# Performance work log

Hardware: AMD Instinct MI355X
Metric: run time of the kernel (lower is better)

Reference implementation:

```python
import jax, jax.numpy as jnp
import numpy as np

EMBED_DIM = 1024
HEADS = 16


def setup_inputs() -> dict:
    key = jax.random.key(0)
    ks = jax.random.split(key, 9)
    d = EMBED_DIM
    s = 1.0 / np.sqrt(d)
    x = jax.random.normal(ks[0], (4, 2048, d), dtype=jnp.float32)
    return {
        "x": x,
        "Wq": jax.random.uniform(ks[1], (d, d), jnp.float32, -s, s),
        "bq": jax.random.uniform(ks[2], (d,), jnp.float32, -s, s),
        "Wk": jax.random.uniform(ks[3], (d, d), jnp.float32, -s, s),
        "bk": jax.random.uniform(ks[4], (d,), jnp.float32, -s, s),
        "Wv": jax.random.uniform(ks[5], (d, d), jnp.float32, -s, s),
        "bv": jax.random.uniform(ks[6], (d,), jnp.float32, -s, s),
        "Wo": jax.random.uniform(ks[7], (d, d), jnp.float32, -s, s),
        "bo": jax.random.uniform(ks[8], (d,), jnp.float32, -s, s),
    }


def reference(x, Wq, bq, Wk, bk, Wv, bv, Wo, bo):
    B, N, C = x.shape
    H = HEADS
    Dh = C // H
    scale = Dh ** (-0.5)
    # Linear projections (torch Linear: x @ W.T + b), split heads -> [B,H,N,Dh]
    def split_heads(t):
        return t.reshape(B, N, H, Dh).transpose(0, 2, 1, 3)
    q = split_heads(x @ Wq.T + bq)
    k = split_heads(x @ Wk.T + bk)
    v = split_heads(x @ Wv.T + bv)
    attn = jnp.einsum('bhnd,bhmd->bhnm', q, k) * scale  # [B,H,N,N]
    attn = jax.nn.softmax(attn, axis=-1)
    # dropout ratio is 0.0 (eval); abs() kept for faithfulness
    out = jnp.einsum('bhnm,bhmd->bhnd', jnp.abs(attn), v)
    out = out.transpose(0, 2, 1, 3).reshape(B, N, C)
    return out @ Wo.T + bo
```

## Files before the change

kernel.cpp:

```cpp
#include <hip/hip_runtime.h>
#include <hip/hip_bf16.h>
#include <cstddef>
#include <cstdint>

namespace {
constexpr int Bn = 4, SEQ = 2048, CDIM = 1024, NH = 16, DH = 64;
constexpr int Mrows = Bn * SEQ;
}

using bf16x8 = __attribute__((ext_vector_type(8))) __bf16;
using f32x4  = __attribute__((ext_vector_type(4))) float;
using f32x16 = __attribute__((ext_vector_type(16))) float;

#define MFMA16(a, b, c) __builtin_amdgcn_mfma_f32_16x16x32_bf16(a, b, c, 0, 0, 0)
#define MFMA32(a, b, c) __builtin_amdgcn_mfma_f32_32x32x16_bf16(a, b, c, 0, 0, 0)

__device__ __forceinline__ void gload_lds16(const __bf16* g, __bf16* l) {
  __builtin_amdgcn_global_load_lds(
      (const __attribute__((address_space(1))) void*)g,
      (__attribute__((address_space(3))) void*)l, 16, 0, 0);
}

__device__ __forceinline__ unsigned pk2(float a, float b) {
  union { __bf16 h[2]; unsigned u; } x;
  x.h[0] = (__bf16)a; x.h[1] = (__bf16)b;
  return x.u;
}

__global__ __launch_bounds__(256) void cast_inputs(
    const float* __restrict__ x, const float* __restrict__ wq,
    const float* __restrict__ wk, const float* __restrict__ wv,
    const float* __restrict__ wo, __bf16* __restrict__ xb,
    __bf16* __restrict__ wall) {
  constexpr int X4 = Mrows * CDIM / 4;
  constexpr int W4 = CDIM * CDIM / 4;
  constexpr int total = X4 + 4 * W4;
  for (int i = blockIdx.x * 256 + threadIdx.x; i < total; i += gridDim.x * 256) {
    const float4* src;
    __bf16* dst;
    int o;
    if (i < X4) {
      src = (const float4*)x; dst = xb; o = i;
    } else {
      int j = i - X4;
      int w = j >> 18;
      o = j & (W4 - 1);
      src = (const float4*)(w == 0 ? wq : w == 1 ? wk : w == 2 ? wv : wo);
      dst = wall + (size_t)w * (CDIM * CDIM);
    }
    float4 v = src[o];
    union { __bf16 h[4]; ushort4 u4; } pk;
    pk.h[0] = (__bf16)v.x; pk.h[1] = (__bf16)v.y;
    pk.h[2] = (__bf16)v.z; pk.h[3] = (__bf16)v.w;
    *(ushort4*)(dst + (size_t)o * 4) = pk.u4;
  }
}

template <int MODE>
__global__ __launch_bounds__(256) void gemm_mfma(
    const __bf16* __restrict__ A, const __bf16* __restrict__ Bw,
    const float* __restrict__ b0, const float* __restrict__ b1,
    const float* __restrict__ b2, __bf16* __restrict__ Qb,
    __bf16* __restrict__ Kb, __bf16* __restrict__ Vb,
    float* __restrict__ Yf) {
  __shared__ __align__(16) __bf16 As[128 * 32];
  __shared__ __align__(16) __bf16 Bs[128 * 32];
  const int tid = threadIdx.x;
  const int lane = tid & 63, w = tid >> 6;
  const int wr = w >> 1, wc = w & 1;
  const int l4 = lane >> 4, l15 = lane & 15;
  const int m0 = blockIdx.y * 128, n0 = blockIdx.x * 128;

  f32x4 acc[4][4] = {};
  const int srow = lane >> 2;
  const int scol = (lane & 3) * 8;

  for (int k0 = 0; k0 < CDIM; k0 += 32) {
    __syncthreads();
#pragma unroll
    for (int u = 0; u < 2; ++u) {
      const int c = w * 2 + u;
      gload_lds16(A + (size_t)(m0 + c * 16 + srow) * CDIM + k0 + scol,
                  &As[c * 512]);
      gload_lds16(Bw + (size_t)(n0 + c * 16 + srow) * CDIM + k0 + scol,
                  &Bs[c * 512]);
    }
    __syncthreads();
    bf16x8 af[4], bfr[4];
#pragma unroll
    for (int i = 0; i < 4; ++i)
      af[i] = *(const bf16x8*)&As[(wr * 64 + i * 16 + l15) * 32 + l4 * 8];
#pragma unroll
    for (int j = 0; j < 4; ++j)
      bfr[j] = *(const bf16x8*)&Bs[(wc * 64 + j * 16 + l15) * 32 + l4 * 8];
#pragma unroll
    for (int i = 0; i < 4; ++i)
#pragma unroll
      for (int j = 0; j < 4; ++j)
        acc[i][j] = MFMA16(af[i], bfr[j], acc[i][j]);
  }

  const int row0 = m0 + wr * 64;
  if (MODE == 0) {
#pragma unroll
    for (int j = 0; j < 4; ++j) {
      const int n = (n0 + wc * 64 + j * 16) + l15;
      const float bias = b0[n];
#pragma unroll
      for (int i = 0; i < 4; ++i) {
        const int mrow = row0 + i * 16 + l4 * 4;
#pragma unroll
        for (int r = 0; r < 4; ++r)
          Yf[(size_t)(mrow + r) * CDIM + n] = acc[i][j][r] + bias;
      }
    }
  } else {
    const int which = n0 >> 10;
    const float* bias = which == 0 ? b0 : which == 1 ? b1 : b2;
    __bf16* Out = which == 0 ? Qb : which == 1 ? Kb : Vb;
    const float scl = which == 0 ? 0.125f : 1.0f;
    const int n0c = n0 & 1023;
#pragma unroll
    for (int j = 0; j < 4; ++j) {
      const int c = n0c + wc * 64 + j * 16 + l15;
      const int h = c >> 6, dh = c & 63;
      const float bias_v = bias[c];
#pragma unroll
      for (int i = 0; i < 4; ++i) {
        const int mrow = row0 + i * 16 + l4 * 4;
#pragma unroll
        for (int r = 0; r < 4; ++r) {
          const int m = mrow + r;
          const int b_ = m >> 11, ns = m & (SEQ - 1);
          Out[((size_t)(b_ * NH + h) * SEQ + ns) * DH + dh] =
              (__bf16)((acc[i][j][r] + bias_v) * scl);
        }
      }
    }
  }
}

__global__ __launch_bounds__(256) void attn_mfma(
    const __bf16* __restrict__ Qg, const __bf16* __restrict__ Kg,
    const __bf16* __restrict__ Vg, __bf16* __restrict__ AO) {
  __shared__ __align__(16) __bf16 vT[2][64][72];
  const int tid = threadIdx.x, lane = tid & 63, w = tid >> 6;
  const int l31 = lane & 31, hi = lane >> 5;
  const int bh = blockIdx.x, qt = blockIdx.y;
  const int b_ = bh >> 4, h_ = bh & 15;

  const __bf16* Qp = Qg + ((size_t)bh * SEQ + qt * 128 + w * 32) * DH;
  const __bf16* Kb = Kg + (size_t)bh * SEQ * DH;
  const __bf16* Vb = Vg + (size_t)bh * SEQ * DH;

  bf16x8 q[4];
#pragma unroll
  for (int t = 0; t < 4; ++t)
    q[t] = *(const bf16x8*)(Qp + (size_t)l31 * DH + t * 16 + hi * 8);

  f32x16 o0 = {}, o1 = {};
  float m_i = -1e30f, l_i = 0.f;

  const int vkey = tid & 63, vdg = (tid >> 6) * 16;

  bf16x8 kfA[8], kfB[8];
  bf16x8 vfA[2], vfB[2];
  auto kload = [&](bf16x8(&kf)[8], int kt) {
#pragma unroll
    for (int c = 0; c < 2; ++c)
#pragma unroll
      for (int t = 0; t < 4; ++t)
        kf[c * 4 + t] = *(const bf16x8*)(
            Kb + ((size_t)kt * 64 + c * 32 + l31) * DH + t * 16 + hi * 8);
  };
  auto vload = [&](bf16x8(&vf)[2], int kt) {
    const __bf16* Vt = Vb + (size_t)kt * 64 * DH;
    vf[0] = *(const bf16x8*)(Vt + (size_t)vkey * DH + vdg);
    vf[1] = *(const bf16x8*)(Vt + (size_t)vkey * DH + vdg + 8);
  };
  kload(kfA, 0);
  vload(vfA, 0);

  auto body = [&](bf16x8(&kc)[8], bf16x8(&kn)[8], bf16x8(&vc)[2],
                  bf16x8(&vn)[2], int kt, int buf) {
    const int ktn = (kt + 1) & 31;
    vload(vn, ktn);
    kload(kn, ktn);
    f32x16 s0 = {}, s1 = {};
    __builtin_amdgcn_s_setprio(1);
#pragma unroll
    for (int t = 0; t < 4; ++t) {
      s0 = MFMA32(kc[t], q[t], s0);
      s1 = MFMA32(kc[4 + t], q[t], s1);
    }
    __builtin_amdgcn_s_setprio(0);
#pragma unroll
    for (int e = 0; e < 8; ++e) vT[buf][vdg + e][vkey] = vc[0][e];
#pragma unroll
    for (int e = 0; e < 8; ++e) vT[buf][vdg + 8 + e][vkey] = vc[1][e];
    __syncthreads();
    float mt[16];
#pragma unroll
    for (int j = 0; j < 16; ++j) mt[j] = fmaxf(s0[j], s1[j]);
#pragma unroll
    for (int st = 8; st > 0; st >>= 1)
#pragma unroll
      for (int j = 0; j < 8; ++j)
        if (j < st) mt[j] = fmaxf(mt[j], mt[j + st]);
    float mx = fmaxf(mt[0], __shfl_xor(mt[0], 32));
    if (!__all(mx <= m_i + 8.0f)) {
      const float mnew = fmaxf(m_i, mx);
      const float alpha = __expf(m_i - mnew);
      m_i = mnew;
      l_i *= alpha;
      o0 *= alpha;
      o1 *= alpha;
    }
    unsigned W0[4][2], W1[4][2];
    float psa[4] = {0.f, 0.f, 0.f, 0.f};
#pragma unroll
    for (int m = 0; m < 4; ++m)
#pragma unroll
      for (int j2 = 0; j2 < 2; ++j2) {
        float a0 = __expf(s0[4 * m + 2 * j2] - m_i);
        float a1 = __expf(s0[4 * m + 2 * j2 + 1] - m_i);
        float b0 = __expf(s1[4 * m + 2 * j2] - m_i);
        float b1 = __expf(s1[4 * m + 2 * j2 + 1] - m_i);
        psa[m] += (a0 + a1) + (b0 + b1);
        W0[m][j2] = pk2(a0, a1);
        W1[m][j2] = pk2(b0, b1);
      }
    float ps = (psa[0] + psa[1]) + (psa[2] + psa[3]);
    ps += __shfl_xor(ps, 32);
    l_i += ps;
    bf16x8 Bp[4];
#pragma unroll
    for (int X = 0; X < 2; ++X)
#pragma unroll
      for (int k2 = 0; k2 < 2; ++k2) {
        union { unsigned u[4]; bf16x8 v; } bb;
#pragma unroll
        for (int j2 = 0; j2 < 2; ++j2) {
          const unsigned a = X ? W1[2 * k2][j2] : W0[2 * k2][j2];
          const unsigned b = X ? W1[2 * k2 + 1][j2] : W0[2 * k2 + 1][j2];
          const unsigned snd = hi ? a : b;
          const unsigned rcv = __shfl_xor(snd, 32);
          bb.u[j2] = hi ? rcv : a;
          bb.u[2 + j2] = hi ? b : rcv;
        }
        Bp[X * 2 + k2] = bb.v;
      }
    __builtin_amdgcn_s_setprio(1);
#pragma unroll
    for (int ks = 0; ks < 4; ++ks) {
      bf16x8 va0 = *(const bf16x8*)&vT[buf][l31][ks * 16 + hi * 8];
      bf16x8 va1 = *(const bf16x8*)&vT[buf][32 + l31][ks * 16 + hi * 8];
      o0 = MFMA32(va0, Bp[ks], o0);
      o1 = MFMA32(va1, Bp[ks], o1);
    }
    __builtin_amdgcn_s_setprio(0);
  };

#pragma unroll 1
  for (int kt2 = 0; kt2 < 16; ++kt2) {
    body(kfA, kfB, vfA, vfB, 2 * kt2, 0);
    body(kfB, kfA, vfB, vfA, 2 * kt2 + 1, 1);
  }

  const float inv = 1.f / l_i;
  const int qglob = qt * 128 + w * 32 + l31;
  __bf16* aorow = AO + ((size_t)(b_ * SEQ) + qglob) * CDIM + h_ * DH;
#pragma unroll
  for (int u = 0; u < 8; ++u) {
    const int dbase = 8 * (u >> 1) + 4 * hi + 2 * (u & 1);
    *(unsigned*)(aorow + dbase) = pk2(o0[2 * u] * inv, o0[2 * u + 1] * inv);
    *(unsigned*)(aorow + 32 + dbase) = pk2(o1[2 * u] * inv, o1[2 * u + 1] * inv);
  }
}

extern "C" void kernel_launch(void* const* d_in, const int* in_sizes, int n_in,
                              void* d_out, int out_size, void* d_ws,
                              size_t ws_size, hipStream_t stream) {
  const float* x  = (const float*)d_in[0];
  const float* Wq = (const float*)d_in[1];
  const float* bq = (const float*)d_in[2];
  const float* Wk = (const float*)d_in[3];
  const float* bk = (const float*)d_in[4];
  const float* Wv = (const float*)d_in[5];
  const float* bv = (const float*)d_in[6];
  const float* Wo = (const float*)d_in[7];
  const float* bo = (const float*)d_in[8];
  float* out = (float*)d_out;

  __bf16* xb   = (__bf16*)d_ws;
  __bf16* wall = xb + (size_t)Mrows * CDIM;
  __bf16* Qb   = wall + (size_t)4 * CDIM * CDIM;
  __bf16* Kb   = Qb + (size_t)Mrows * CDIM;
  __bf16* Vb   = Kb + (size_t)Mrows * CDIM;
  __bf16* AO   = Vb + (size_t)Mrows * CDIM;

  cast_inputs<<<2048, 256, 0, stream>>>(x, Wq, Wk, Wv, Wo, xb, wall);
  gemm_mfma<1><<<dim3(24, 64), 256, 0, stream>>>(xb, wall, bq, bk, bv, Qb, Kb,
                                                 Vb, nullptr);
  attn_mfma<<<dim3(Bn * NH, SEQ / 128), 256, 0, stream>>>(Qb, Kb, Vb, AO);
  gemm_mfma<0><<<dim3(8, 64), 256, 0, stream>>>(
      AO, wall + (size_t)3 * CDIM * CDIM, bo, nullptr, nullptr, nullptr,
      nullptr, nullptr, out);
}
```

Before: 349.5 us.

## Write V pre-transposed from QKV GEMM and use single-wave LDS-free attention blocks

The QKV projection epilogue now writes V in a transposed [B,H,Dh,SEQ] layout with packed stores, so the attention kernel can load V operands straight from global memory without staging and transposing them through LDS behind a barrier. Attention blocks shrink to a single wave handling 32 queries, and the explicit K/V register double-buffering and priority hints are removed. The softmax moves to the native exp2 instruction, with the Q scale folded to include log2(e). In exchange, K and V are re-read from global memory or cache by every wave rather than shared across four waves, and there is no explicit prefetch of the next tile.

New measurement: 440.9 us. +26.2%, slower.

```diff
diff --git a/kernel.cpp b/kernel.cpp
--- a/kernel.cpp
+++ b/kernel.cpp
@@ -117,41 +117,57 @@
   } else {
     const int which = n0 >> 10;
     const float* bias = which == 0 ? b0 : which == 1 ? b1 : b2;
-    __bf16* Out = which == 0 ? Qb : which == 1 ? Kb : Vb;
-    const float scl = which == 0 ? 0.125f : 1.0f;
     const int n0c = n0 & 1023;
-#pragma unroll
-    for (int j = 0; j < 4; ++j) {
-      const int c = n0c + wc * 64 + j * 16 + l15;
-      const int h = c >> 6, dh = c & 63;
-      const float bias_v = bias[c];
-#pragma unroll
-      for (int i = 0; i < 4; ++i) {
-        const int mrow = row0 + i * 16 + l4 * 4;
-#pragma unroll
-        for (int r = 0; r < 4; ++r) {
-          const int m = mrow + r;
-          const int b_ = m >> 11, ns = m & (SEQ - 1);
-          Out[((size_t)(b_ * NH + h) * SEQ + ns) * DH + dh] =
-              (__bf16)((acc[i][j][r] + bias_v) * scl);
+    if (which == 2) {
+#pragma unroll
+      for (int j = 0; j < 4; ++j) {
+        const int c = n0c + wc * 64 + j * 16 + l15;
+        const int h = c >> 6, dh = c & 63;
+        const float bias_v = bias[c];
+#pragma unroll
+        for (int i = 0; i < 4; ++i) {
+          const int mrow = row0 + i * 16 + l4 * 4;
+          const int b_ = mrow >> 11, ns = mrow & (SEQ - 1);
+          __bf16* p = Vb + ((size_t)(b_ * NH + h) * DH + dh) * SEQ + ns;
+          *(unsigned*)p = pk2(acc[i][j][0] + bias_v, acc[i][j][1] + bias_v);
+          *(unsigned*)(p + 2) = pk2(acc[i][j][2] + bias_v, acc[i][j][3] + bias_v);
         }
       }
-    }
-  }
-}
-
-__global__ __launch_bounds__(256) void attn_mfma(
+    } else {
+      __bf16* Out = which == 0 ? Qb : Kb;
+      const float scl = which == 0 ? 0.18033688f : 1.0f;
+#pragma unroll
+      for (int j = 0; j < 4; ++j) {
+        const int c = n0c + wc * 64 + j * 16 + l15;
+        const int h = c >> 6, dh = c & 63;
+        const float bias_v = bias[c];
+#pragma unroll
+        for (int i = 0; i < 4; ++i) {
+          const int mrow = row0 + i * 16 + l4 * 4;
+#pragma unroll
+          for (int r = 0; r < 4; ++r) {
+            const int m = mrow + r;
+            const int b_ = m >> 11, ns = m & (SEQ - 1);
+            Out[((size_t)(b_ * NH + h) * SEQ + ns) * DH + dh] =
+                (__bf16)((acc[i][j][r] + bias_v) * scl);
+          }
+        }
+      }
+    }
+  }
+}
+
+__global__ __launch_bounds__(64) void attn_mfma(
     const __bf16* __restrict__ Qg, const __bf16* __restrict__ Kg,
-    const __bf16* __restrict__ Vg, __bf16* __restrict__ AO) {
-  __shared__ __align__(16) __bf16 vT[2][64][72];
-  const int tid = threadIdx.x, lane = tid & 63, w = tid >> 6;
+    const __bf16* __restrict__ VTg, __bf16* __restrict__ AO) {
+  const int lane = threadIdx.x & 63;
   const int l31 = lane & 31, hi = lane >> 5;
   const int bh = blockIdx.x, qt = blockIdx.y;
   const int b_ = bh >> 4, h_ = bh & 15;
 
-  const __bf16* Qp = Qg + ((size_t)bh * SEQ + qt * 128 + w * 32) * DH;
+  const __bf16* Qp = Qg + ((size_t)bh * SEQ + qt * 32) * DH;
   const __bf16* Kb = Kg + (size_t)bh * SEQ * DH;
-  const __bf16* Vb = Vg + (size_t)bh * SEQ * DH;
+  const __bf16* VT = VTg + (size_t)bh * DH * SEQ;
 
   bf16x8 q[4];
 #pragma unroll
@@ -161,44 +177,21 @@
   f32x16 o0 = {}, o1 = {};
   float m_i = -1e30f, l_i = 0.f;
 
-  const int vkey = tid & 63, vdg = (tid >> 6) * 16;
-
-  bf16x8 kfA[8], kfB[8];
-  bf16x8 vfA[2], vfB[2];
-  auto kload = [&](bf16x8(&kf)[8], int kt) {
-#pragma unroll
-    for (int c = 0; c < 2; ++c)
-#pragma unroll
-      for (int t = 0; t < 4; ++t)
-        kf[c * 4 + t] = *(const bf16x8*)(
-            Kb + ((size_t)kt * 64 + c * 32 + l31) * DH + t * 16 + hi * 8);
-  };
-  auto vload = [&](bf16x8(&vf)[2], int kt) {
-    const __bf16* Vt = Vb + (size_t)kt * 64 * DH;
-    vf[0] = *(const bf16x8*)(Vt + (size_t)vkey * DH + vdg);
-    vf[1] = *(const bf16x8*)(Vt + (size_t)vkey * DH + vdg + 8);
-  };
-  kload(kfA, 0);
-  vload(vfA, 0);
-
-  auto body = [&](bf16x8(&kc)[8], bf16x8(&kn)[8], bf16x8(&vc)[2],
-                  bf16x8(&vn)[2], int kt, int buf) {
-    const int ktn = (kt + 1) & 31;
-    vload(vn, ktn);
-    kload(kn, ktn);
+#pragma unroll 2
+  for (int kt = 0; kt < 32; ++kt) {
+    const __bf16* Kt = Kb + (size_t)kt * 64 * DH;
+    const __bf16* Vt = VT + kt * 64;
     f32x16 s0 = {}, s1 = {};
-    __builtin_amdgcn_s_setprio(1);
 #pragma unroll
     for (int t = 0; t < 4; ++t) {
-      s0 = MFMA32(kc[t], q[t], s0);
-      s1 = MFMA32(kc[4 + t], q[t], s1);
-    }
-    __builtin_amdgcn_s_setprio(0);
-#pragma unroll
-    for (int e = 0; e < 8; ++e) vT[buf][vdg + e][vkey] = vc[0][e];
-#pragma unroll
-    for (int e = 0; e < 8; ++e) vT[buf][vdg + 8 + e][vkey] = vc[1][e];
-    __syncthreads();
+      bf16x8 ka = *(const bf16x8*)(Kt + (size_t)l31 * DH + t * 16 + hi * 8);
+      s0 = MFMA32(ka, q[t], s0);
+    }
+#pragma unroll
+    for (int t = 0; t < 4; ++t) {
+      bf16x8 kc = *(const bf16x8*)(Kt + (size_t)(32 + l31) * DH + t * 16 + hi * 8);
+      s1 = MFMA32(kc, q[t], s1);
+    }
     float mt[16];
 #pragma unroll
     for (int j = 0; j < 16; ++j) mt[j] = fmaxf(s0[j], s1[j]);
@@ -210,7 +203,7 @@
     float mx = fmaxf(mt[0], __shfl_xor(mt[0], 32));
     if (!__all(mx <= m_i + 8.0f)) {
       const float mnew = fmaxf(m_i, mx);
-      const float alpha = __expf(m_i - mnew);
+      const float alpha = __builtin_amdgcn_exp2f(m_i - mnew);
       m_i = mnew;
       l_i *= alpha;
       o0 *= alpha;
@@ -222,10 +215,10 @@
     for (int m = 0; m < 4; ++m)
 #pragma unroll
       for (int j2 = 0; j2 < 2; ++j2) {
-        float a0 = __expf(s0[4 * m + 2 * j2] - m_i);
-        float a1 = __expf(s0[4 * m + 2 * j2 + 1] - m_i);
-        float b0 = __expf(s1[4 * m + 2 * j2] - m_i);
-        float b1 = __expf(s1[4 * m + 2 * j2 + 1] - m_i);
+        float a0 = __builtin_amdgcn_exp2f(s0[4 * m + 2 * j2] - m_i);
+        float a1 = __builtin_amdgcn_exp2f(s0[4 * m + 2 * j2 + 1] - m_i);
+        float b0 = __builtin_amdgcn_exp2f(s1[4 * m + 2 * j2] - m_i);
+        float b1 = __builtin_amdgcn_exp2f(s1[4 * m + 2 * j2 + 1] - m_i);
         psa[m] += (a0 + a1) + (b0 + b1);
         W0[m][j2] = pk2(a0, a1);
         W1[m][j2] = pk2(b0, b1);
@@ -250,25 +243,18 @@
         }
         Bp[X * 2 + k2] = bb.v;
       }
-    __builtin_amdgcn_s_setprio(1);
 #pragma unroll
     for (int ks = 0; ks < 4; ++ks) {
-      bf16x8 va0 = *(const bf16x8*)&vT[buf][l31][ks * 16 + hi * 8];
-      bf16x8 va1 = *(const bf16x8*)&vT[buf][32 + l31][ks * 16 + hi * 8];
+      bf16x8 va0 = *(const bf16x8*)(Vt + (size_t)l31 * SEQ + ks * 16 + hi * 8);
+      bf16x8 va1 =
+          *(const bf16x8*)(Vt + (size_t)(32 + l31) * SEQ + ks * 16 + hi * 8);
       o0 = MFMA32(va0, Bp[ks], o0);
       o1 = MFMA32(va1, Bp[ks], o1);
     }
-    __builtin_amdgcn_s_setprio(0);
-  };
-
-#pragma unroll 1
-  for (int kt2 = 0; kt2 < 16; ++kt2) {
-    body(kfA, kfB, vfA, vfB, 2 * kt2, 0);
-    body(kfB, kfA, vfB, vfA, 2 * kt2 + 1, 1);
   }
 
   const float inv = 1.f / l_i;
-  const int qglob = qt * 128 + w * 32 + l31;
+  const int qglob = qt * 32 + l31;
   __bf16* aorow = AO + ((size_t)(b_ * SEQ) + qglob) * CDIM + h_ * DH;
 #pragma unroll
   for (int u = 0; u < 8; ++u) {
@@ -296,13 +282,13 @@
   __bf16* wall = xb + (size_t)Mrows * CDIM;
   __bf16* Qb   = wall + (size_t)4 * CDIM * CDIM;
   __bf16* Kb   = Qb + (size_t)Mrows * CDIM;
-  __bf16* Vb   = Kb + (size_t)Mrows * CDIM;
-  __bf16* AO   = Vb + (size_t)Mrows * CDIM;
+  __bf16* Vt   = Kb + (size_t)Mrows * CDIM;
+  __bf16* AO   = Vt + (size_t)Mrows * CDIM;
 
   cast_inputs<<<2048, 256, 0, stream>>>(x, Wq, Wk, Wv, Wo, xb, wall);
   gemm_mfma<1><<<dim3(24, 64), 256, 0, stream>>>(xb, wall, bq, bk, bv, Qb, Kb,
-                                                 Vb, nullptr);
-  attn_mfma<<<dim3(Bn * NH, SEQ / 128), 256, 0, stream>>>(Qb, Kb, Vb, AO);
+                                                 Vt, nullptr);
+  attn_mfma<<<dim3(Bn * NH, SEQ / 32), 64, 0, stream>>>(Qb, Kb, Vt, AO);
   gemm_mfma<0><<<dim3(8, 64), 256, 0, stream>>>(
       AO, wall + (size_t)3 * CDIM * CDIM, bo, nullptr, nullptr, nullptr,
       nullptr, nullptr, out);
```
